# Kernel optimization log

Hardware: AMD Instinct MI355X
Metric: run time of the kernel (lower is better)

## Reference

```python
import jax, jax.numpy as jnp
import numpy as np

EPS = 1e-8  # torch F.cosine_similarity clamps norms to eps=1e-8


def setup_inputs() -> dict:
    key = jax.random.key(0)
    k1, k2 = jax.random.split(key)
    token_embeddings = jax.random.normal(k1, (32, 512, 768), dtype=jnp.float32)
    projection = jax.random.normal(k2, (2048, 768), dtype=jnp.float32)
    return {"token_embeddings": token_embeddings, "projection": projection}


def reference(token_embeddings, projection):
    # cosine_similarity(x[b,s,1,d], p[1,1,o,d], dim=-1) == normalize(x) @ normalize(p).T
    # with norms clamped to EPS, then mean over sequence dim -> [B, O]
    x_norm = jnp.maximum(jnp.linalg.norm(token_embeddings, axis=-1, keepdims=True), EPS)
    p_norm = jnp.maximum(jnp.linalg.norm(projection, axis=-1, keepdims=True), EPS)
    xn = token_embeddings / x_norm          # [B, S, D]
    pn = projection / p_norm                # [O, D]
    cos = jnp.einsum("bsd,od->bso", xn, pn)  # [B, S, O]
    sentence_embedding = cos.mean(axis=1)    # [B, O]
    return sentence_embedding
```

## Files before the change

### kernel.cpp

```cpp
#include <hip/hip_runtime.h>

#define EPS_F 1e-8f

static constexpr int B = 32;
static constexpr int S = 512;
static constexpr int D = 768;
static constexpr int O = 2048;

static constexpr int ROWS_PER_BLOCK = 16;
static constexpr int CHUNKS = S / ROWS_PER_BLOCK;

__global__ __launch_bounds__(256)
void mean_norm_partial_kernel(const float* __restrict__ x, float* __restrict__ part) {
    const int bid  = blockIdx.x;
    const int b    = bid / CHUNKS;
    const int c    = bid % CHUNKS;
    const int wave = threadIdx.x >> 6;
    const int lane = threadIdx.x & 63;

    const float* xb = x + ((size_t)b * S + (size_t)c * ROWS_PER_BLOCK) * D;

    float racc[12];
#pragma unroll
    for (int j = 0; j < 12; ++j) racc[j] = 0.0f;

#pragma unroll
    for (int rr = 0; rr < ROWS_PER_BLOCK / 4; ++rr) {
        const int r = rr * 4 + wave;
        const float* row = xb + (size_t)r * D;
        const float4 v0 = *(const float4*)(row + 0 * 256 + lane * 4);
        const float4 v1 = *(const float4*)(row + 1 * 256 + lane * 4);
        const float4 v2 = *(const float4*)(row + 2 * 256 + lane * 4);
        float ssq = v0.x * v0.x + v0.y * v0.y + v0.z * v0.z + v0.w * v0.w
                  + v1.x * v1.x + v1.y * v1.y + v1.z * v1.z + v1.w * v1.w
                  + v2.x * v2.x + v2.y * v2.y + v2.z * v2.z + v2.w * v2.w;
#pragma unroll
        for (int off = 1; off < 64; off <<= 1) ssq += __shfl_xor(ssq, off);
        const float inv = 1.0f / fmaxf(sqrtf(ssq), EPS_F);
        racc[0]  += v0.x * inv;  racc[1]  += v0.y * inv;
        racc[2]  += v0.z * inv;  racc[3]  += v0.w * inv;
        racc[4]  += v1.x * inv;  racc[5]  += v1.y * inv;
        racc[6]  += v1.z * inv;  racc[7]  += v1.w * inv;
        racc[8]  += v2.x * inv;  racc[9]  += v2.y * inv;
        racc[10] += v2.z * inv;  racc[11] += v2.w * inv;
    }

    __shared__ float lacc[4][D];
#pragma unroll
    for (int k = 0; k < 3; ++k) {
        float4 v = make_float4(racc[k * 4 + 0], racc[k * 4 + 1],
                               racc[k * 4 + 2], racc[k * 4 + 3]);
        *(float4*)&lacc[wave][k * 256 + lane * 4] = v;
    }
    __syncthreads();

    if (threadIdx.x < D / 4) {
        const int d4 = threadIdx.x * 4;
        float4 v;
        v.x = lacc[0][d4 + 0] + lacc[1][d4 + 0] + lacc[2][d4 + 0] + lacc[3][d4 + 0];
        v.y = lacc[0][d4 + 1] + lacc[1][d4 + 1] + lacc[2][d4 + 1] + lacc[3][d4 + 1];
        v.z = lacc[0][d4 + 2] + lacc[1][d4 + 2] + lacc[2][d4 + 2] + lacc[3][d4 + 2];
        v.w = lacc[0][d4 + 3] + lacc[1][d4 + 3] + lacc[2][d4 + 3] + lacc[3][d4 + 3];
        *(float4*)(part + (size_t)bid * D + d4) = v;
    }
}

__global__ __launch_bounds__(256)
void reduce_partials_kernel(const float* __restrict__ part, float* __restrict__ y) {
    const int b    = blockIdx.x / 3;
    const int dseg = blockIdx.x % 3;
    const int d    = dseg * 256 + threadIdx.x;

    const float* pb = part + (size_t)b * CHUNKS * D + d;
    float s = 0.0f;
#pragma unroll
    for (int c = 0; c < CHUNKS; ++c) s += pb[(size_t)c * D];
    y[b * D + d] = s * (1.0f / (float)S);
}

static constexpr int OJ = 4;
static constexpr int HALF = D / 2;

__global__ __launch_bounds__(256)
void proj_kernel(const float* __restrict__ p, const float* __restrict__ y,
                 float* __restrict__ out) {
    const int o0  = blockIdx.x * OJ;
    const int tid = threadIdx.x;
    const int h   = tid & 1;
    const int oj  = (tid >> 1) & (OJ - 1);
    const int b   = tid >> 3;

    const float* prow = p + (size_t)(o0 + oj) * D + h * HALF;
    const float* yrow = y + (size_t)b * D + h * HALF;

    float dot = 0.0f, sp = 0.0f;
#pragma unroll 8
    for (int d = 0; d < HALF; d += 4) {
        const float4 pv = *(const float4*)(prow + d);
        const float4 yv = *(const float4*)(yrow + d);
        dot += pv.x * yv.x + pv.y * yv.y + pv.z * yv.z + pv.w * yv.w;
        sp  += pv.x * pv.x + pv.y * pv.y + pv.z * pv.z + pv.w * pv.w;
    }

    dot += __shfl_xor(dot, 1);
    sp  += __shfl_xor(sp, 1);

    if (h == 0) {
        out[b * O + (o0 + oj)] = dot / fmaxf(sqrtf(sp), EPS_F);
    }
}

extern "C" void kernel_launch(void* const* d_in, const int* in_sizes, int n_in,
                              void* d_out, int out_size, void* d_ws, size_t ws_size,
                              hipStream_t stream) {
    const float* x = (const float*)d_in[0];
    const float* p = (const float*)d_in[1];
    float* out = (float*)d_out;

    float* y    = (float*)d_ws;
    float* part = y + (size_t)B * D;

    mean_norm_partial_kernel<<<B * CHUNKS, 256, 0, stream>>>(x, part);
    reduce_partials_kernel<<<B * 3, 256, 0, stream>>>(part, y);
    proj_kernel<<<O / OJ, 256, 0, stream>>>(p, y, out);
}
```

Baseline: 119.9 us.

## Batch row loads in mean-norm kernel and stage y in LDS for projection

The partial mean-norm kernel now issues all four rows' loads before any reduction, so more memory requests are in flight per wave. The projection kernel is restructured: each block stages 16 batch rows of y into shared memory and each wave owns one output row of p, normalizing it once and reusing it across 16 batches. Without this, every thread re-reads p and y from global memory. The cost is a 48KB LDS footprint per block and 16 wave-wide shuffle reductions per wave, which may limit occupancy.

```diff
diff --git a/kernel.cpp b/kernel.cpp
--- a/kernel.cpp
+++ b/kernel.cpp
@@ -20,30 +20,34 @@
 
     const float* xb = x + ((size_t)b * S + (size_t)c * ROWS_PER_BLOCK) * D;
 
+    float vv[4][12];
+#pragma unroll
+    for (int rr = 0; rr < 4; ++rr) {
+        const float* row = xb + (size_t)(rr * 4 + wave) * D + lane * 4;
+#pragma unroll
+        for (int k = 0; k < 3; ++k) {
+            const float4 t = *(const float4*)(row + k * 256);
+            vv[rr][k * 4 + 0] = t.x; vv[rr][k * 4 + 1] = t.y;
+            vv[rr][k * 4 + 2] = t.z; vv[rr][k * 4 + 3] = t.w;
+        }
+    }
+
+    float inv[4];
+#pragma unroll
+    for (int rr = 0; rr < 4; ++rr) {
+        float ssq = 0.0f;
+#pragma unroll
+        for (int j = 0; j < 12; ++j) ssq += vv[rr][j] * vv[rr][j];
+#pragma unroll
+        for (int off = 1; off < 64; off <<= 1) ssq += __shfl_xor(ssq, off);
+        inv[rr] = 1.0f / fmaxf(sqrtf(ssq), EPS_F);
+    }
+
     float racc[12];
 #pragma unroll
-    for (int j = 0; j < 12; ++j) racc[j] = 0.0f;
-
-#pragma unroll
-    for (int rr = 0; rr < ROWS_PER_BLOCK / 4; ++rr) {
-        const int r = rr * 4 + wave;
-        const float* row = xb + (size_t)r * D;
-        const float4 v0 = *(const float4*)(row + 0 * 256 + lane * 4);
-        const float4 v1 = *(const float4*)(row + 1 * 256 + lane * 4);
-        const float4 v2 = *(const float4*)(row + 2 * 256 + lane * 4);
-        float ssq = v0.x * v0.x + v0.y * v0.y + v0.z * v0.z + v0.w * v0.w
-                  + v1.x * v1.x + v1.y * v1.y + v1.z * v1.z + v1.w * v1.w
-                  + v2.x * v2.x + v2.y * v2.y + v2.z * v2.z + v2.w * v2.w;
-#pragma unroll
-        for (int off = 1; off < 64; off <<= 1) ssq += __shfl_xor(ssq, off);
-        const float inv = 1.0f / fmaxf(sqrtf(ssq), EPS_F);
-        racc[0]  += v0.x * inv;  racc[1]  += v0.y * inv;
-        racc[2]  += v0.z * inv;  racc[3]  += v0.w * inv;
-        racc[4]  += v1.x * inv;  racc[5]  += v1.y * inv;
-        racc[6]  += v1.z * inv;  racc[7]  += v1.w * inv;
-        racc[8]  += v2.x * inv;  racc[9]  += v2.y * inv;
-        racc[10] += v2.z * inv;  racc[11] += v2.w * inv;
-    }
+    for (int j = 0; j < 12; ++j)
+        racc[j] = vv[0][j] * inv[0] + vv[1][j] * inv[1]
+                + vv[2][j] * inv[2] + vv[3][j] * inv[3];
 
     __shared__ float lacc[4][D];
 #pragma unroll
@@ -78,35 +82,70 @@
     y[b * D + d] = s * (1.0f / (float)S);
 }
 
-static constexpr int OJ = 4;
-static constexpr int HALF = D / 2;
+static constexpr int BH = 16;
+static constexpr int OW = 8;
 
-__global__ __launch_bounds__(256)
+__global__ __launch_bounds__(512)
 void proj_kernel(const float* __restrict__ p, const float* __restrict__ y,
                  float* __restrict__ out) {
-    const int o0  = blockIdx.x * OJ;
-    const int tid = threadIdx.x;
-    const int h   = tid & 1;
-    const int oj  = (tid >> 1) & (OJ - 1);
-    const int b   = tid >> 3;
+    __shared__ float ylds[BH * D];
 
-    const float* prow = p + (size_t)(o0 + oj) * D + h * HALF;
-    const float* yrow = y + (size_t)b * D + h * HALF;
+    const int half = blockIdx.y;
+    const int tid  = threadIdx.x;
 
-    float dot = 0.0f, sp = 0.0f;
-#pragma unroll 8
-    for (int d = 0; d < HALF; d += 4) {
-        const float4 pv = *(const float4*)(prow + d);
-        const float4 yv = *(const float4*)(yrow + d);
-        dot += pv.x * yv.x + pv.y * yv.y + pv.z * yv.z + pv.w * yv.w;
-        sp  += pv.x * pv.x + pv.y * pv.y + pv.z * pv.z + pv.w * pv.w;
+    const float* ysrc = y + (size_t)half * BH * D;
+#pragma unroll
+    for (int i = 0; i < (BH * D) / (512 * 4); ++i) {
+        const int f4 = i * 512 + tid;
+        *(float4*)&ylds[f4 * 4] = *(const float4*)&ysrc[f4 * 4];
+    }
+    __syncthreads();
+
+    const int wave = tid >> 6;
+    const int lane = tid & 63;
+    const int o    = blockIdx.x * OW + wave;
+
+    const float* prow = p + (size_t)o * D + lane * 4;
+    float4 pv[3];
+#pragma unroll
+    for (int k = 0; k < 3; ++k) pv[k] = *(const float4*)(prow + k * 256);
+
+    float ssq = 0.0f;
+#pragma unroll
+    for (int k = 0; k < 3; ++k)
+        ssq += pv[k].x * pv[k].x + pv[k].y * pv[k].y
+             + pv[k].z * pv[k].z + pv[k].w * pv[k].w;
+#pragma unroll
+    for (int off = 1; off < 64; off <<= 1) ssq += __shfl_xor(ssq, off);
+    const float inv = 1.0f / fmaxf(sqrtf(ssq), EPS_F);
+#pragma unroll
+    for (int k = 0; k < 3; ++k) {
+        pv[k].x *= inv; pv[k].y *= inv; pv[k].z *= inv; pv[k].w *= inv;
     }
 
-    dot += __shfl_xor(dot, 1);
-    sp  += __shfl_xor(sp, 1);
+    float tot[BH];
+#pragma unroll
+    for (int b = 0; b < BH; ++b) {
+        const float* yb = &ylds[b * D + lane * 4];
+        float acc = 0.0f;
+#pragma unroll
+        for (int k = 0; k < 3; ++k) {
+            const float4 yv = *(const float4*)(yb + k * 256);
+            acc += pv[k].x * yv.x + pv[k].y * yv.y
+                 + pv[k].z * yv.z + pv[k].w * yv.w;
+        }
+        tot[b] = acc;
+    }
+#pragma unroll
+    for (int b = 0; b < BH; ++b) {
+#pragma unroll
+        for (int off = 1; off < 64; off <<= 1) tot[b] += __shfl_xor(tot[b], off);
+    }
 
-    if (h == 0) {
-        out[b * O + (o0 + oj)] = dot / fmaxf(sqrtf(sp), EPS_F);
+    if (lane == 0) {
+#pragma unroll
+        for (int b = 0; b < BH; ++b)
+            out[(size_t)(half * BH + b) * O + o] = tot[b];
     }
 }
 
@@ -122,5 +161,5 @@
 
     mean_norm_partial_kernel<<<B * CHUNKS, 256, 0, stream>>>(x, part);
     reduce_partials_kernel<<<B * 3, 256, 0, stream>>>(part, y);
-    proj_kernel<<<O / OJ, 256, 0, stream>>>(p, y, out);
+    proj_kernel<<<dim3(O / OW, 2), 512, 0, stream>>>(p, y, out);
 }
```

Result: faster. 96.58 us (median of 2 runs) (-19.4%).
